# Optimization experiments

Measured on AMD Instinct MI355X. Metric: run time of the kernel, lower is better.

Reference implementation:

```python
import jax, jax.numpy as jnp
import numpy as np

B, L, H, NT = 16, 2048, 512, 8
HEAD_H = max(32, H // 2)
OUT = 2 * H + NT
LN_EPS = 1e-5


def setup_inputs() -> dict:
    key = jax.random.key(0)
    ks = jax.random.split(key, 32)
    def w(i, shape):
        fan_in = shape[0] if len(shape) > 1 else shape[0]
        return jax.random.normal(ks[i], shape, jnp.float32) / np.sqrt(fan_in)
    z = lambda shape: jnp.zeros(shape, jnp.float32)
    return {
        "x": jax.random.normal(ks[0], (B, L, 2), jnp.float32),
        "t": jax.random.uniform(ks[1], (B, L, 1), jnp.float32),
        "Wt1": w(2, (1, NT)), "bt1": z((NT,)),
        "Wt2": w(3, (NT, NT)), "bt2": z((NT,)),
        "Wpf": w(4, (2 + NT, H)), "bpf": z((H,)),
        "Wpb": w(5, (2 + NT, H)), "bpb": z((H,)),
        "Wzf": w(6, (H, H)), "bzf": z((H,)),
        "Whf": w(7, (H, H)), "bhf": z((H,)),
        "Wzb": w(8, (H, H)), "bzb": z((H,)),
        "Whb": w(9, (H, H)), "bhb": z((H,)),
        "ln_g": jnp.ones((OUT,), jnp.float32), "ln_b": z((OUT,)),
        "time_scale": jnp.array(5.0, jnp.float32),
        "Wg1": w(10, (OUT, HEAD_H)), "bg1": z((HEAD_H,)),
        "Wg2": w(11, (HEAD_H, 1)), "bg2": z((1,)),
    }


def _mingru_states(xc, Wp, bp, Wz, bz, Wh, bh):
    """Run minGRU over xc (B,L,D); return h_prev states: out[:,ti] = h before step ti."""
    inp = xc @ Wp + bp                      # (B,L,H)
    zg = jax.nn.sigmoid(inp @ Wz + bz)
    h_tilde = jnp.tanh(inp @ Wh + bh)
    a = 1.0 - zg                            # decay
    b = zg * h_tilde                        # input injection
    def step(h, ab):
        h = ab[0] * h + ab[1]
        return h, h
    h0 = jnp.zeros((xc.shape[0], Wh.shape[1]), xc.dtype)
    _, hs = jax.lax.scan(step, h0, (jnp.moveaxis(a, 1, 0), jnp.moveaxis(b, 1, 0)))
    hs = jnp.moveaxis(hs, 0, 1)             # (B,L,H), hs[:,ti] = h after step ti
    # Original stores h_prev at each position -> shift right with zero prefix.
    return jnp.concatenate([jnp.zeros_like(hs[:, :1]), hs[:, :-1]], axis=1)


def reference(x, t, Wt1, bt1, Wt2, bt2, Wpf, bpf, Wpb, bpb,
              Wzf, bzf, Whf, bhf, Wzb, bzb, Whb, bhb,
              ln_g, ln_b, time_scale, Wg1, bg1, Wg2, bg2):
    t_enc = jnp.maximum(t @ Wt1 + bt1, 0.0) @ Wt2 + bt2   # (B,L,NT)
    xc = jnp.concatenate([x, t_enc], axis=-1)              # (B,L,2+NT)
    h_fwd = _mingru_states(xc, Wpf, bpf, Wzf, bzf, Whf, bhf)
    # Backward direction: run scan on time-reversed input, then flip back.
    h_bwd = _mingru_states(xc[:, ::-1], Wpb, bpb, Wzb, bzb, Whb, bhb)[:, ::-1]
    h_bi = jnp.concatenate([h_fwd, h_bwd, t_enc], axis=-1)  # (B,L,OUT)
    mu = jnp.mean(h_bi, axis=-1, keepdims=True)
    var = jnp.mean(jnp.square(h_bi - mu), axis=-1, keepdims=True)
    h_bi = (h_bi - mu) * jax.lax.rsqrt(var + LN_EPS) * ln_g + ln_b
    h_bi = jnp.concatenate([h_bi[..., :-NT], h_bi[..., -NT:] * time_scale], axis=-1)
    hid = jax.nn.gelu(h_bi @ Wg1 + bg1, approximate=False)
    return hid @ Wg2 + bg2                                  # (B,L,1)
```

## Files before the change

kernel.cpp:

```cpp
#include <hip/hip_runtime.h>
#include <hip/hip_bf16.h>
#include <math.h>

#define B_    16
#define L_    2048
#define H_    512
#define NT_   8
#define OUT_  1032
#define HEAD_ 256
#define CH_   16
#define CL_   (L_/CH_)
#define NWS_  1152

#define ACH_  136
#define ASTR_ (ACH_*8)
#define RB5_  32

typedef short bf16x8 __attribute__((ext_vector_type(8)));
typedef float f32x4  __attribute__((ext_vector_type(4)));

__device__ __forceinline__ float b2f(unsigned short u) {
    union { unsigned int u32; float f; } v; v.u32 = ((unsigned int)u) << 16; return v.f;
}
__device__ __forceinline__ unsigned short f2b(float f) {
    __hip_bfloat16 h = __float2bfloat16(f);
    return *reinterpret_cast<unsigned short*>(&h);
}
__device__ __forceinline__ float sigmoid_f(float x) {
    return 1.f / (1.f + exp2f(-1.44269504f * x));
}
__device__ __forceinline__ float tanh_f(float x) {
    float e = exp2f(2.88539008f * x);
    return 1.f - 2.f / (e + 1.f);
}
__device__ __forceinline__ float gelu_f(float g) {
    float u  = 0.70710678118654752f * g;
    float ax = fabsf(u);
    float t  = 1.f / (1.f + 0.3275911f * ax);
    float poly = ((((1.061405429f*t - 1.453152027f)*t + 1.421413741f)*t
                   - 0.284496736f)*t + 0.254829592f)*t;
    float e  = exp2f(-1.44269504f * ax * ax);
    float er = 1.f - poly * e;
    er = (u < 0.f) ? -er : er;
    return 0.5f * g * (1.f + er);
}

__global__ __launch_bounds__(256) void kT(const float* __restrict__ in,
                                          unsigned short* __restrict__ out,
                                          int R, int C, int RP)
{
    __shared__ float tile[32][33];
    int c0 = blockIdx.x * 32, r0 = blockIdx.y * 32;
    int tx = threadIdx.x & 31, ty = threadIdx.x >> 5;
    #pragma unroll
    for (int j = 0; j < 32; j += 8) {
        int r = r0 + ty + j, c = c0 + tx;
        tile[ty + j][tx] = (r < R && c < C) ? in[(size_t)r*C + c] : 0.f;
    }
    __syncthreads();
    #pragma unroll
    for (int j = 0; j < 32; j += 8) {
        int c = c0 + ty + j, r = r0 + tx;
        if (c < C && r < RP) out[(size_t)c*RP + r] = f2b(tile[tx][ty + j]);
    }
}

__global__ __launch_bounds__(256) void kP(const float* __restrict__ Wg1,
                                          uint4* __restrict__ P)
{
    int idx = blockIdx.x*256 + threadIdx.x;
    if (idx >= 33*1024) return;
    int kb = idx >> 10;
    int rem = idx & 1023;
    int c  = rem >> 2;
    int kg = rem & 3;
    int k0 = kb*32 + kg*8;
    unsigned short o[8];
    #pragma unroll
    for (int j = 0; j < 8; j++) {
        int k = k0 + j;
        o[j] = (k < OUT_) ? f2b(Wg1[(size_t)k*HEAD_ + c]) : (unsigned short)0;
    }
    P[idx] = *(const uint4*)o;
}

__global__ __launch_bounds__(256) void k1_tenc_inp(
    const float* __restrict__ x, const float* __restrict__ t,
    const float* __restrict__ Wt1, const float* __restrict__ bt1,
    const float* __restrict__ Wt2, const float* __restrict__ bt2,
    const float* __restrict__ Wp, const float* __restrict__ bp,
    float* __restrict__ t_enc,
    unsigned short* __restrict__ inp)
{
    int wv = threadIdx.x >> 6, lane = threadIdx.x & 63;
    size_t row = (size_t)blockIdx.x*4 + wv;
    float tv = t[row];
    float r1[NT_], te[NT_];
    #pragma unroll
    for (int k = 0; k < NT_; k++) r1[k] = fmaxf(tv*Wt1[k] + bt1[k], 0.f);
    #pragma unroll
    for (int j = 0; j < NT_; j++) {
        float a = bt2[j];
        #pragma unroll
        for (int k = 0; k < NT_; k++) a = fmaf(r1[k], Wt2[k*NT_+j], a);
        te[j] = a;
    }
    if (lane < NT_) t_enc[row*NT_ + lane] = te[lane];
    float x0 = x[row*2+0], x1 = x[row*2+1];
    int c0 = lane*8;
    float af[8];
    #pragma unroll
    for (int j = 0; j < 8; j++) {
        int c = c0 + j;
        af[j] = fmaf(x0, Wp[c], fmaf(x1, Wp[H_+c], bp[c]));
    }
    #pragma unroll
    for (int k = 0; k < NT_; k++) {
        #pragma unroll
        for (int j = 0; j < 8; j++)
            af[j] = fmaf(te[k], Wp[(2+k)*H_+c0+j], af[j]);
    }
    unsigned short of[8];
    #pragma unroll
    for (int j = 0; j < 8; j++) of[j] = f2b(af[j]);
    *(uint4*)&inp[row*H_ + c0] = *(const uint4*)of;
}

__global__ __launch_bounds__(256) void k3g(
    const unsigned short* __restrict__ inp,
    const unsigned short* __restrict__ WT,
    unsigned short* __restrict__ zt_out,
    int nwg)
{
    __shared__ __align__(16) unsigned short As[128*40];
    __shared__ __align__(16) unsigned short Bs[128*40];
    int tid = threadIdx.x;
    int lane = tid & 63, w = tid >> 6;
    int wm = w >> 1, wn = w & 1;
    int kg = lane >> 4, lr = lane & 15;

    int bid = blockIdx.x;
    int cpx = nwg >> 3;
    int tile = (bid & 7) * cpx + (bid >> 3);
    int row0 = (tile >> 3) * 128;
    int n0   = (tile & 7) * 128;

    f32x4 acc[4][4];
    #pragma unroll
    for (int m = 0; m < 4; m++)
        #pragma unroll
        for (int n = 0; n < 4; n++) acc[m][n] = (f32x4){0.f,0.f,0.f,0.f};

    int ar = tid >> 1, aseg = tid & 1;

    uint4 va0, va1, vb0, vb1;
    {
        const uint4* ga = (const uint4*)&inp[(size_t)(row0+ar)*H_ + aseg*16];
        va0 = ga[0]; va1 = ga[1];
        const uint4* gb = (const uint4*)&WT[(size_t)(n0+ar)*H_ + aseg*16];
        vb0 = gb[0]; vb1 = gb[1];
    }

    for (int k0 = 0; k0 < H_; k0 += 32) {
        __syncthreads();
        *(uint4*)&As[ar*40 + aseg*16]     = va0;
        *(uint4*)&As[ar*40 + aseg*16 + 8] = va1;
        *(uint4*)&Bs[ar*40 + aseg*16]     = vb0;
        *(uint4*)&Bs[ar*40 + aseg*16 + 8] = vb1;
        __syncthreads();
        if (k0 + 32 < H_) {
            const uint4* ga = (const uint4*)&inp[(size_t)(row0+ar)*H_ + k0+32 + aseg*16];
            va0 = ga[0]; va1 = ga[1];
            const uint4* gb = (const uint4*)&WT[(size_t)(n0+ar)*H_ + k0+32 + aseg*16];
            vb0 = gb[0]; vb1 = gb[1];
        }
        bf16x8 af[4], bf[4];
        #pragma unroll
        for (int m = 0; m < 4; m++)
            af[m] = *(const bf16x8*)&As[(wm*64 + m*16 + lr)*40 + kg*8];
        #pragma unroll
        for (int n = 0; n < 4; n++)
            bf[n] = *(const bf16x8*)&Bs[(wn*64 + n*16 + lr)*40 + kg*8];
        #pragma unroll
        for (int m = 0; m < 4; m++)
            #pragma unroll
            for (int n = 0; n < 4; n++)
                acc[m][n] = __builtin_amdgcn_mfma_f32_16x16x32_bf16(af[m], bf[n], acc[m][n], 0, 0, 0);
    }

    #pragma unroll
    for (int m = 0; m < 4; m++)
        #pragma unroll
        for (int n = 0; n < 4; n++) {
            int colg = n0 + wn*64 + n*16 + lr;
            #pragma unroll
            for (int r = 0; r < 4; r++) {
                int rowg = row0 + wm*64 + m*16 + kg*4 + r;
                zt_out[(size_t)rowg*NWS_ + colg] = f2b(acc[m][n][r]);
            }
        }
}

__global__ __launch_bounds__(256) void k4a(
    unsigned short* __restrict__ ATF, unsigned short* __restrict__ ATB,
    const float* __restrict__ bzf, const float* __restrict__ bhf,
    const float* __restrict__ bzb, const float* __restrict__ bhb,
    float* __restrict__ Scar, float* __restrict__ Pcar, int nb)
{
    int g = blockIdx.x*256 + threadIdx.x;
    int col   = g & (H_-1);
    int chunk = (g >> 9) & (CH_-1);
    int rest  = g >> 13;
    int bb    = rest % nb;
    int dir   = rest / nb;
    unsigned short* AT = dir ? ATB : ATF;
    float bzv = (dir ? bzb : bzf)[col];
    float bhv = (dir ? bhb : bhf)[col];
    size_t base = (size_t)bb * L_ * NWS_ + col;
    float h = 0.f, pp = 1.f;
    if (dir == 0) {
        int lo = chunk * CL_;
        for (int p = 0; p < CL_; p += 8) {
            unsigned short zv[8], hv[8];
            #pragma unroll
            for (int j = 0; j < 8; j++) {
                size_t idx = base + (size_t)(lo+p+j)*NWS_;
                zv[j] = AT[idx]; hv[j] = AT[idx + H_];
            }
            #pragma unroll
            for (int j = 0; j < 8; j++) {
                size_t idx = base + (size_t)(lo+p+j)*NWS_;
                float zg = sigmoid_f(b2f(zv[j]) + bzv);
                float a  = 1.f - zg;
                float bg = zg * tanh_f(b2f(hv[j]) + bhv);
                AT[idx]      = f2b(h);
                AT[idx + H_] = f2b(pp);
                h = fmaf(a, h, bg);
                pp *= a;
            }
        }
    } else {
        int hi = chunk * CL_ + CL_ - 1;
        for (int p = 0; p < CL_; p += 8) {
            unsigned short zv[8], hv[8];
            #pragma unroll
            for (int j = 0; j < 8; j++) {
                size_t idx = base + (size_t)(hi-p-j)*NWS_;
                zv[j] = AT[idx]; hv[j] = AT[idx + H_];
            }
            #pragma unroll
            for (int j = 0; j < 8; j++) {
                size_t idx = base + (size_t)(hi-p-j)*NWS_;
                float zg = sigmoid_f(b2f(zv[j]) + bzv);
                float a  = 1.f - zg;
                float bg = zg * tanh_f(b2f(hv[j]) + bhv);
                AT[idx]      = f2b(h);
                AT[idx + H_] = f2b(pp);
                h = fmaf(a, h, bg);
                pp *= a;
            }
        }
    }
    int ci = ((dir*nb + bb)*CH_ + chunk)*H_ + col;
    Scar[ci] = h; Pcar[ci] = pp;
}

__global__ __launch_bounds__(256) void k4b(
    const float* __restrict__ Scar, const float* __restrict__ Pcar,
    float* __restrict__ Hstart, int nb)
{
    int g = blockIdx.x*256 + threadIdx.x;
    int col  = g & (H_-1);
    int rest = g >> 9;
    int bb   = rest % nb;
    int dir  = rest / nb;
    int baseci = (dir*nb + bb)*CH_;
    float h = 0.f;
    if (dir == 0) {
        for (int c = 0; c < CH_; c++) {
            int ci = (baseci + c)*H_ + col;
            Hstart[ci] = h;
            h = Scar[ci] + Pcar[ci]*h;
        }
    } else {
        for (int c = CH_-1; c >= 0; c--) {
            int ci = (baseci + c)*H_ + col;
            Hstart[ci] = h;
            h = Scar[ci] + Pcar[ci]*h;
        }
    }
}

__global__ __launch_bounds__(256) void k5_fused(
    const unsigned short* __restrict__ ATF, const unsigned short* __restrict__ ATB,
    const float* __restrict__ Hstart,
    const float* __restrict__ tenc,
    const float* __restrict__ ln_g, const float* __restrict__ ln_b,
    const float* __restrict__ tsp,
    const uint4* __restrict__ P,
    const float* __restrict__ bg1, const float* __restrict__ Wg2,
    const float* __restrict__ bg2,
    float* __restrict__ out, int nb)
{
    __shared__ __align__(16) unsigned short A[RB5_*ASTR_];
    __shared__ float red[4][RB5_];
    int tid = threadIdx.x, lane = tid & 63, wv = tid >> 6;
    int kg = lane >> 4, lr = lane & 15;
    int row0 = blockIdx.x * RB5_;
    float ts = tsp[0];

    int bb    = row0 >> 11;
    int chunk = (row0 & (L_-1)) >> 7;
    int cif = (bb*CH_ + chunk)*H_;
    int cib = ((nb + bb)*CH_ + chunk)*H_;
    int c0 = lane*8;
    float4 hfa = *(const float4*)&Hstart[cif + c0];
    float4 hfb = *(const float4*)&Hstart[cif + c0 + 4];
    float4 hba = *(const float4*)&Hstart[cib + c0];
    float4 hbb = *(const float4*)&Hstart[cib + c0 + 4];
    float h0f[8] = {hfa.x,hfa.y,hfa.z,hfa.w,hfb.x,hfb.y,hfb.z,hfb.w};
    float h0b[8] = {hba.x,hba.y,hba.z,hba.w,hbb.x,hbb.y,hbb.z,hbb.w};

    float gf[8], bf_[8], gb_[8], bb_[8];
    #pragma unroll
    for (int j = 0; j < 8; j++) {
        gf[j]  = ln_g[c0+j];     bf_[j] = ln_b[c0+j];
        gb_[j] = ln_g[H_+c0+j];  bb_[j] = ln_b[H_+c0+j];
    }
    float gt = 0.f, bt = 0.f;
    if (lane < NT_) { gt = ln_g[2*H_+lane]; bt = ln_b[2*H_+lane]; }

    size_t rowBase = (size_t)(row0 + wv*8) * NWS_;
    uint4 cSF = *(const uint4*)&ATF[rowBase + c0];
    uint4 cPF = *(const uint4*)&ATF[rowBase + H_ + c0];
    uint4 cSB = *(const uint4*)&ATB[rowBase + c0];
    uint4 cPB = *(const uint4*)&ATB[rowBase + H_ + c0];

    #pragma unroll
    for (int i = 0; i < 8; i++) {
        int r = wv*8 + i;
        size_t row = (size_t)row0 + r;
        uint4 SF = cSF, PF = cPF, SB = cSB, PB = cPB;
        if (i < 7) {
            size_t rb2 = rowBase + (size_t)(i+1)*NWS_;
            cSF = *(const uint4*)&ATF[rb2 + c0];
            cPF = *(const uint4*)&ATF[rb2 + H_ + c0];
            cSB = *(const uint4*)&ATB[rb2 + c0];
            cPB = *(const uint4*)&ATB[rb2 + H_ + c0];
        }
        const unsigned short* sf = (const unsigned short*)&SF;
        const unsigned short* pf = (const unsigned short*)&PF;
        const unsigned short* sb = (const unsigned short*)&SB;
        const unsigned short* pb = (const unsigned short*)&PB;
        float fv[8], bv[8];
        float S = 0.f, Q = 0.f;
        #pragma unroll
        for (int j = 0; j < 8; j++) {
            fv[j] = fmaf(b2f(pf[j]), h0f[j], b2f(sf[j]));
            S += fv[j]; Q += fv[j]*fv[j];
            bv[j] = fmaf(b2f(pb[j]), h0b[j], b2f(sb[j]));
            S += bv[j]; Q += bv[j]*bv[j];
        }
        float tv = 0.f;
        if (lane < NT_) { tv = tenc[row*NT_ + lane]; S += tv; Q += tv*tv; }
        #pragma unroll
        for (int off = 32; off > 0; off >>= 1) {
            S += __shfl_xor(S, off, 64);
            Q += __shfl_xor(Q, off, 64);
        }
        float mu = S * (1.f/1032.f);
        float rs = rsqrtf(Q * (1.f/1032.f) - mu*mu + 1e-5f);
        int key = r & 7;
        unsigned short o[8];
        #pragma unroll
        for (int j = 0; j < 8; j++) o[j] = f2b((fv[j]-mu)*rs*gf[j] + bf_[j]);
        *(uint4*)&A[r*ASTR_ + ((lane ^ key)*8)] = *(const uint4*)o;
        #pragma unroll
        for (int j = 0; j < 8; j++) o[j] = f2b((bv[j]-mu)*rs*gb_[j] + bb_[j]);
        *(uint4*)&A[r*ASTR_ + (((64+lane) ^ key)*8)] = *(const uint4*)o;
        if (lane < NT_) {
            A[r*ASTR_ + ((128 ^ key)*8) + lane] =
                f2b(((tv-mu)*rs*gt + bt) * ts);
        } else {
            int cc = 128 + (lane >> 3);
            A[r*ASTR_ + ((cc ^ key)*8) + (lane & 7)] = 0;
        }
    }
    __syncthreads();

    f32x4 acc[2][4];
    #pragma unroll
    for (int m = 0; m < 2; m++)
        #pragma unroll
        for (int n = 0; n < 4; n++) acc[m][n] = (f32x4){0.f,0.f,0.f,0.f};

    const uint4* Pw = P + wv*256 + lr*4 + kg;
    int keyA = lr & 7;

#define LOADB(v0,v1,v2,v3,KB) do { \
        const uint4* q_ = Pw + (KB)*1024; \
        v0 = *(const bf16x8*)&q_[0]; \
        v1 = *(const bf16x8*)&q_[64]; \
        v2 = *(const bf16x8*)&q_[128]; \
        v3 = *(const bf16x8*)&q_[192]; \
    } while(0)
#define LDSA0(KB) (*(const bf16x8*)&A[lr*ASTR_      + ((((KB)*4+kg) ^ keyA)*8)])
#define LDSA1(KB) (*(const bf16x8*)&A[(16+lr)*ASTR_ + ((((KB)*4+kg) ^ keyA)*8)])
#define MFMA8(v0,v1,v2,v3,a0_,a1_) do { \
        acc[0][0] = __builtin_amdgcn_mfma_f32_16x16x32_bf16(a0_, v0, acc[0][0],0,0,0); \
        acc[0][1] = __builtin_amdgcn_mfma_f32_16x16x32_bf16(a0_, v1, acc[0][1],0,0,0); \
        acc[0][2] = __builtin_amdgcn_mfma_f32_16x16x32_bf16(a0_, v2, acc[0][2],0,0,0); \
        acc[0][3] = __builtin_amdgcn_mfma_f32_16x16x32_bf16(a0_, v3, acc[0][3],0,0,0); \
        acc[1][0] = __builtin_amdgcn_mfma_f32_16x16x32_bf16(a1_, v0, acc[1][0],0,0,0); \
        acc[1][1] = __builtin_amdgcn_mfma_f32_16x16x32_bf16(a1_, v1, acc[1][1],0,0,0); \
        acc[1][2] = __builtin_amdgcn_mfma_f32_16x16x32_bf16(a1_, v2, acc[1][2],0,0,0); \
        acc[1][3] = __builtin_amdgcn_mfma_f32_16x16x32_bf16(a1_, v3, acc[1][3],0,0,0); \
    } while(0)

    bf16x8 a0,a1,a2,a3, d0,d1,d2,d3, e0,e1,e2,e3;
    LOADB(a0,a1,a2,a3, 0);
    LOADB(d0,d1,d2,d3, 1);
    LOADB(e0,e1,e2,e3, 2);
    for (int kb = 0; kb < 30; kb += 3) {
        bf16x8 af0, af1;
        af0 = LDSA0(kb);   af1 = LDSA1(kb);
        MFMA8(a0,a1,a2,a3, af0, af1);
        LOADB(a0,a1,a2,a3, kb+3);
        af0 = LDSA0(kb+1); af1 = LDSA1(kb+1);
        MFMA8(d0,d1,d2,d3, af0, af1);
        LOADB(d0,d1,d2,d3, kb+4);
        af0 = LDSA0(kb+2); af1 = LDSA1(kb+2);
        MFMA8(e0,e1,e2,e3, af0, af1);
        LOADB(e0,e1,e2,e3, kb+5);
    }
    {
        bf16x8 af0, af1;
        af0 = LDSA0(30); af1 = LDSA1(30);
        MFMA8(a0,a1,a2,a3, af0, af1);
        af0 = LDSA0(31); af1 = LDSA1(31);
        MFMA8(d0,d1,d2,d3, af0, af1);
        af0 = LDSA0(32); af1 = LDSA1(32);
        MFMA8(e0,e1,e2,e3, af0, af1);
    }
#undef LOADB
#undef LDSA0
#undef LDSA1
#undef MFMA8

    float rsum[2][4] = {{0.f,0.f,0.f,0.f},{0.f,0.f,0.f,0.f}};
    #pragma unroll
    for (int n = 0; n < 4; n++) {
        int colg = wv*64 + n*16 + lr;
        float bgv = bg1[colg], w2v = Wg2[colg];
        #pragma unroll
        for (int m = 0; m < 2; m++)
            #pragma unroll
            for (int r = 0; r < 4; r++) {
                float gv = gelu_f(acc[m][n][r] + bgv);
                rsum[m][r] = fmaf(gv, w2v, rsum[m][r]);
            }
    }
    #pragma unroll
    for (int off = 1; off < 16; off <<= 1)
        #pragma unroll
        for (int m = 0; m < 2; m++)
            #pragma unroll
            for (int r = 0; r < 4; r++)
                rsum[m][r] += __shfl_xor(rsum[m][r], off, 64);
    if (lr == 0) {
        #pragma unroll
        for (int m = 0; m < 2; m++)
            #pragma unroll
            for (int r = 0; r < 4; r++)
                red[wv][m*16 + kg*4 + r] = rsum[m][r];
    }
    __syncthreads();
    if (tid < RB5_)
        out[row0 + tid] = red[0][tid] + red[1][tid] + red[2][tid] + red[3][tid] + bg2[0];
}

extern "C" void kernel_launch(void* const* d_in, const int* in_sizes, int n_in,
                              void* d_out, int out_size, void* d_ws, size_t ws_size,
                              hipStream_t stream)
{
    const float* x    = (const float*)d_in[0];
    const float* t    = (const float*)d_in[1];
    const float* Wt1  = (const float*)d_in[2];
    const float* bt1  = (const float*)d_in[3];
    const float* Wt2  = (const float*)d_in[4];
    const float* bt2  = (const float*)d_in[5];
    const float* Wpf  = (const float*)d_in[6];
    const float* bpf  = (const float*)d_in[7];
    const float* Wpb  = (const float*)d_in[8];
    const float* bpb  = (const float*)d_in[9];
    const float* Wzf  = (const float*)d_in[10];
    const float* bzf  = (const float*)d_in[11];
    const float* Whf  = (const float*)d_in[12];
    const float* bhf  = (const float*)d_in[13];
    const float* Wzb  = (const float*)d_in[14];
    const float* bzb  = (const float*)d_in[15];
    const float* Whb  = (const float*)d_in[16];
    const float* bhb  = (const float*)d_in[17];
    const float* ln_g = (const float*)d_in[18];
    const float* ln_b = (const float*)d_in[19];
    const float* tsc  = (const float*)d_in[20];
    const float* Wg1  = (const float*)d_in[21];
    const float* bg1  = (const float*)d_in[22];
    const float* Wg2  = (const float*)d_in[23];
    const float* bg2  = (const float*)d_in[24];
    float* out = (float*)d_out;

    char* p = (char*)d_ws;
    auto carve = [&](size_t bytes) -> char* {
        char* q = p; p += (bytes + 255) & ~(size_t)255; return q;
    };

    unsigned short* WTf = (unsigned short*)carve((size_t)2*H_*H_*2);
    unsigned short* WTb = (unsigned short*)carve((size_t)2*H_*H_*2);
    uint4*          Pg  = (uint4*)carve((size_t)33*1024*16);

    const size_t perBatch = (size_t)L_*H_*2
                          + (size_t)L_*NWS_*2*2
                          + (size_t)L_*NT_*4
                          + (size_t)CH_*H_*4*3*2;
    size_t fixedUsed = (size_t)(p - (char*)d_ws) + 64*1024;
    int NB = B_;
    while (NB > 1 && fixedUsed + (size_t)NB*perBatch > ws_size) NB >>= 1;

    unsigned short* inp = (unsigned short*)carve((size_t)NB*L_*H_*2);
    unsigned short* ATF = (unsigned short*)carve((size_t)NB*L_*NWS_*2);
    unsigned short* ATB = (unsigned short*)carve((size_t)NB*L_*NWS_*2);
    float* tenc   = (float*)carve((size_t)NB*L_*NT_*4);
    float* Scar   = (float*)carve((size_t)2*NB*CH_*H_*4);
    float* Pcar   = (float*)carve((size_t)2*NB*CH_*H_*4);
    float* Hstart = (float*)carve((size_t)2*NB*CH_*H_*4);

    {
        dim3 g(H_/32, H_/32);
        kT<<<g, 256, 0, stream>>>(Wzf, WTf,         H_, H_, H_);
        kT<<<g, 256, 0, stream>>>(Whf, WTf + H_*H_, H_, H_, H_);
        kT<<<g, 256, 0, stream>>>(Wzb, WTb,         H_, H_, H_);
        kT<<<g, 256, 0, stream>>>(Whb, WTb + H_*H_, H_, H_, H_);
        kP<<<132, 256, 0, stream>>>(Wg1, Pg);
    }

    for (int b0 = 0; b0 < B_; b0 += NB) {
        int rows = NB * L_;
        int nwg3 = (rows/128) * 8;

        k1_tenc_inp<<<rows/4, 256, 0, stream>>>(
            x + (size_t)b0*L_*2, t + (size_t)b0*L_,
            Wt1, bt1, Wt2, bt2, Wpf, bpf, tenc, inp);
        k3g<<<nwg3, 256, 0, stream>>>(inp, WTf, ATF, nwg3);

        k1_tenc_inp<<<rows/4, 256, 0, stream>>>(
            x + (size_t)b0*L_*2, t + (size_t)b0*L_,
            Wt1, bt1, Wt2, bt2, Wpb, bpb, tenc, inp);
        k3g<<<nwg3, 256, 0, stream>>>(inp, WTb, ATB, nwg3);

        int scanThreads = 2*NB*H_*CH_;
        k4a<<<scanThreads/256, 256, 0, stream>>>(ATF, ATB, bzf, bhf, bzb, bhb,
                                                 Scar, Pcar, NB);
        k4b<<<(2*NB*H_)/256, 256, 0, stream>>>(Scar, Pcar, Hstart, NB);

        k5_fused<<<rows/RB5_, 256, 0, stream>>>(
            ATF, ATB, Hstart, tenc, ln_g, ln_b, tsc,
            Pg, bg1, Wg2, bg2, out + (size_t)b0*L_, NB);
    }
}
```

Baseline: 288.7 us.

## Fuse forward and backward input projections and gate GEMMs into single launches

The input-projection kernel now computes both forward and backward projections in one pass, writing two separate buffers, so the shared time encoding and input loads happen once. The gate GEMM is launched once over twice as many tiles, with each tile choosing its direction, which removes two launches and gives a larger grid. k5_fused also gets a launch-bounds occupancy hint of 2 blocks per CU. The extra input buffer raises workspace needs per batch, which may shrink the batch-chunk size when workspace is limited.

```diff
diff --git a/kernel.cpp b/kernel.cpp
--- a/kernel.cpp
+++ b/kernel.cpp
@@ -88,9 +88,10 @@
     const float* __restrict__ x, const float* __restrict__ t,
     const float* __restrict__ Wt1, const float* __restrict__ bt1,
     const float* __restrict__ Wt2, const float* __restrict__ bt2,
-    const float* __restrict__ Wp, const float* __restrict__ bp,
+    const float* __restrict__ Wpf, const float* __restrict__ bpf,
+    const float* __restrict__ Wpb, const float* __restrict__ bpb,
     float* __restrict__ t_enc,
-    unsigned short* __restrict__ inp)
+    unsigned short* __restrict__ inp_f, unsigned short* __restrict__ inp_b)
 {
     int wv = threadIdx.x >> 6, lane = threadIdx.x & 63;
     size_t row = (size_t)blockIdx.x*4 + wv;
@@ -108,29 +109,36 @@
     if (lane < NT_) t_enc[row*NT_ + lane] = te[lane];
     float x0 = x[row*2+0], x1 = x[row*2+1];
     int c0 = lane*8;
-    float af[8];
+    float af[8], ab[8];
     #pragma unroll
     for (int j = 0; j < 8; j++) {
         int c = c0 + j;
-        af[j] = fmaf(x0, Wp[c], fmaf(x1, Wp[H_+c], bp[c]));
+        af[j] = fmaf(x0, Wpf[c], fmaf(x1, Wpf[H_+c], bpf[c]));
+        ab[j] = fmaf(x0, Wpb[c], fmaf(x1, Wpb[H_+c], bpb[c]));
     }
     #pragma unroll
     for (int k = 0; k < NT_; k++) {
         #pragma unroll
-        for (int j = 0; j < 8; j++)
-            af[j] = fmaf(te[k], Wp[(2+k)*H_+c0+j], af[j]);
-    }
-    unsigned short of[8];
-    #pragma unroll
-    for (int j = 0; j < 8; j++) of[j] = f2b(af[j]);
-    *(uint4*)&inp[row*H_ + c0] = *(const uint4*)of;
+        for (int j = 0; j < 8; j++) {
+            af[j] = fmaf(te[k], Wpf[(2+k)*H_+c0+j], af[j]);
+            ab[j] = fmaf(te[k], Wpb[(2+k)*H_+c0+j], ab[j]);
+        }
+    }
+    unsigned short of[8], ob[8];
+    #pragma unroll
+    for (int j = 0; j < 8; j++) { of[j] = f2b(af[j]); ob[j] = f2b(ab[j]); }
+    *(uint4*)&inp_f[row*H_ + c0] = *(const uint4*)of;
+    *(uint4*)&inp_b[row*H_ + c0] = *(const uint4*)ob;
 }
 
 __global__ __launch_bounds__(256) void k3g(
-    const unsigned short* __restrict__ inp,
-    const unsigned short* __restrict__ WT,
-    unsigned short* __restrict__ zt_out,
-    int nwg)
+    const unsigned short* __restrict__ inpF,
+    const unsigned short* __restrict__ inpB,
+    const unsigned short* __restrict__ WTf,
+    const unsigned short* __restrict__ WTb,
+    unsigned short* __restrict__ ATF,
+    unsigned short* __restrict__ ATB,
+    int nwg, int halfTiles)
 {
     __shared__ __align__(16) unsigned short As[128*40];
     __shared__ __align__(16) unsigned short Bs[128*40];
@@ -142,8 +150,13 @@
     int bid = blockIdx.x;
     int cpx = nwg >> 3;
     int tile = (bid & 7) * cpx + (bid >> 3);
-    int row0 = (tile >> 3) * 128;
-    int n0   = (tile & 7) * 128;
+    int dir  = tile >= halfTiles;
+    int lt   = dir ? (tile - halfTiles) : tile;
+    int row0 = (lt >> 3) * 128;
+    int n0   = (lt & 7) * 128;
+    const unsigned short* inp = dir ? inpB : inpF;
+    const unsigned short* WT  = dir ? WTb : WTf;
+    unsigned short* zt_out    = dir ? ATB : ATF;
 
     f32x4 acc[4][4];
     #pragma unroll
@@ -291,7 +304,7 @@
     }
 }
 
-__global__ __launch_bounds__(256) void k5_fused(
+__global__ __launch_bounds__(256, 2) void k5_fused(
     const unsigned short* __restrict__ ATF, const unsigned short* __restrict__ ATB,
     const float* __restrict__ Hstart,
     const float* __restrict__ tenc,
@@ -519,7 +532,7 @@
     unsigned short* WTb = (unsigned short*)carve((size_t)2*H_*H_*2);
     uint4*          Pg  = (uint4*)carve((size_t)33*1024*16);
 
-    const size_t perBatch = (size_t)L_*H_*2
+    const size_t perBatch = (size_t)L_*H_*2*2
                           + (size_t)L_*NWS_*2*2
                           + (size_t)L_*NT_*4
                           + (size_t)CH_*H_*4*3*2;
@@ -527,7 +540,8 @@
     int NB = B_;
     while (NB > 1 && fixedUsed + (size_t)NB*perBatch > ws_size) NB >>= 1;
 
-    unsigned short* inp = (unsigned short*)carve((size_t)NB*L_*H_*2);
+    unsigned short* inpF = (unsigned short*)carve((size_t)NB*L_*H_*2);
+    unsigned short* inpB = (unsigned short*)carve((size_t)NB*L_*H_*2);
     unsigned short* ATF = (unsigned short*)carve((size_t)NB*L_*NWS_*2);
     unsigned short* ATB = (unsigned short*)carve((size_t)NB*L_*NWS_*2);
     float* tenc   = (float*)carve((size_t)NB*L_*NT_*4);
@@ -546,17 +560,16 @@
 
     for (int b0 = 0; b0 < B_; b0 += NB) {
         int rows = NB * L_;
-        int nwg3 = (rows/128) * 8;
+        int halfTiles = (rows/128) * 8;
+        int nwg3 = 2 * halfTiles;
 
         k1_tenc_inp<<<rows/4, 256, 0, stream>>>(
             x + (size_t)b0*L_*2, t + (size_t)b0*L_,
-            Wt1, bt1, Wt2, bt2, Wpf, bpf, tenc, inp);
-        k3g<<<nwg3, 256, 0, stream>>>(inp, WTf, ATF, nwg3);
-
-        k1_tenc_inp<<<rows/4, 256, 0, stream>>>(
-            x + (size_t)b0*L_*2, t + (size_t)b0*L_,
-            Wt1, bt1, Wt2, bt2, Wpb, bpb, tenc, inp);
-        k3g<<<nwg3, 256, 0, stream>>>(inp, WTb, ATB, nwg3);
+            Wt1, bt1, Wt2, bt2, Wpf, bpf, Wpb, bpb,
+            tenc, inpF, inpB);
+
+        k3g<<<nwg3, 256, 0, stream>>>(inpF, inpB, WTf, WTb, ATF, ATB,
+                                      nwg3, halfTiles);
 
         int scanThreads = 2*NB*H_*CH_;
         k4a<<<scanThreads/256, 256, 0, stream>>>(ATF, ATB, bzf, bhf, bzb, bhb,
```

New measurement: 274.8 us. 1.05x faster.
